# Kernel tuning notes

Measured on AMD Instinct MI355X. Metric: run time of the kernel, lower is better.

Reference implementation:

```python
import jax, jax.numpy as jnp
import numpy as np

EPS = 1e-5

def _layer_norm(x, gamma, beta):
    # LayerNorm over the last two dims [C, 128], matching nn.LayerNorm([C, 128])
    mean = jnp.mean(x, axis=(-2, -1), keepdims=True)
    var = jnp.var(x, axis=(-2, -1), keepdims=True)
    return (x - mean) * jax.lax.rsqrt(var + EPS) * gamma + beta


def setup_inputs() -> dict:
    key = jax.random.key(0)
    ks = jax.random.split(key, 7)
    B, C, N, L = 64, 1024, 128, 512
    W_SCALE = 0.02  # keep pre-softmax logits / activations in a sane range
    return {
        "X_in": jax.random.normal(ks[0], (B, C, N), jnp.float32),
        "T": jax.random.normal(ks[1], (B, C, L), jnp.float32),
        "Wq": jax.random.normal(ks[2], (C, C), jnp.float32) * W_SCALE,
        "Wk": jax.random.normal(ks[3], (C, C), jnp.float32) * W_SCALE,
        "Wv": jax.random.normal(ks[4], (C, C), jnp.float32) * W_SCALE,
        "Wf1": jax.random.normal(ks[5], (C, C), jnp.float32) * W_SCALE,
        "Wf2": jax.random.normal(ks[6], (C, C), jnp.float32) * W_SCALE,
        "gamma": jnp.ones((C, N), jnp.float32),
        "beta": jnp.zeros((C, N), jnp.float32),
    }


def reference(X_in, T, Wq, Wk, Wv, Wf1, Wf2, gamma, beta):
    C = Wq.shape[1]  # feature_map_cs (intended value of the buggy X_in.weight.shape[1])
    # 1x1 Conv1d == per-position channel matmul: weight [out, in]
    q = jnp.einsum('oc,bcn->bon', Wq, X_in)      # [B, C, N]
    k = jnp.einsum('oc,bcl->bol', Wk, T)         # [B, C, L]
    sim = jnp.einsum('bcn,bcl->bnl', q, k) / jnp.sqrt(jnp.float32(C))  # [B, N, L]
    attn = jax.nn.softmax(sim, axis=2)           # softmax over tokens L
    v = jnp.einsum('oc,bcl->bol', Wv, T)         # [B, C, L]
    ctx = jnp.einsum('bcl,bnl->bcn', v, attn)    # [B, C, N] == bmm(values, attn^T)
    X_out = _layer_norm(X_in + ctx, gamma, beta)
    h = jax.nn.relu(jnp.einsum('oc,bcn->bon', Wf1, X_out))
    ffn = jnp.einsum('oc,bcn->bon', Wf2, h)
    return _layer_norm(X_out + ffn, gamma, beta)
```

## Files before the change

kernel.cpp:

```cpp
#include <hip/hip_runtime.h>


using bf16   = __bf16;
using bf16x2 = __attribute__((ext_vector_type(2))) __bf16;
using bf16x4 = __attribute__((ext_vector_type(4))) __bf16;
using bf16x8 = __attribute__((ext_vector_type(8))) __bf16;
using f32x4  = __attribute__((ext_vector_type(4))) float;

static constexpr int  Bb = 64;
static constexpr int  Cc = 1024;
static constexpr int  Nn = 128;
static constexpr int  Ll = 512;
static constexpr long long PLANE = (long long)Cc * Nn;
static constexpr float INV_PLANE = 1.0f / 131072.0f;

__device__ __forceinline__ void gload_lds16(const void* g, void* l) {
    __builtin_amdgcn_global_load_lds(
        (__attribute__((address_space(1))) void*)g,
        (__attribute__((address_space(3))) void*)l,
        16, 0, 0);
}

__global__ void cast_w3(const float* __restrict__ a, const float* __restrict__ b,
                        const float* __restrict__ c,
                        bf16* __restrict__ oa, bf16* __restrict__ ob, bf16* __restrict__ oc) {
    const float* in; bf16* out;
    switch (blockIdx.y) {
        case 0: in = a; out = oa; break;
        case 1: in = b; out = ob; break;
        default: in = c; out = oc; break;
    }
    int i = blockIdx.x * 256 + threadIdx.x;
    float4 v = reinterpret_cast<const float4*>(in)[i];
    bf16x4 o = { (bf16)v.x, (bf16)v.y, (bf16)v.z, (bf16)v.w };
    reinterpret_cast<bf16x4*>(out)[i] = o;
}

template <bool DUAL>
__global__ void transpose_cast_f(const float* __restrict__ in, bf16* __restrict__ outT,
                                 bf16* __restrict__ outS, int R, int S) {
    __shared__ float tile[64][65];
    long long plane = (long long)R * S;
    in   += (long long)blockIdx.z * plane;
    outT += (long long)blockIdx.z * plane;
    if (DUAL) outS += (long long)blockIdx.z * plane;
    int s0 = blockIdx.x * 64, r0 = blockIdx.y * 64;
    int t = threadIdx.x;
    int rl = t >> 4;
    int sc = (t & 15) * 4;
    #pragma unroll
    for (int p = 0; p < 4; ++p) {
        int r = p * 16 + rl;
        float4 v = *(const float4*)(in + (long long)(r0 + r) * S + s0 + sc);
        *(float4*)&tile[r][sc] = v;
        if (DUAL) {
            bf16x4 o = { (bf16)v.x, (bf16)v.y, (bf16)v.z, (bf16)v.w };
            *(bf16x4*)(outS + (long long)(r0 + r) * S + s0 + sc) = o;
        }
    }
    __syncthreads();
    int sb = t >> 3;
    int rg = (t & 7) * 8;
    #pragma unroll
    for (int p = 0; p < 2; ++p) {
        int s = sb + p * 32;
        bf16x8 o;
        #pragma unroll
        for (int j = 0; j < 8; ++j) o[j] = (bf16)tile[rg + j][s];
        *(bf16x8*)(outT + (long long)(s0 + s) * R + r0 + rg) = o;
    }
}

__global__ void transpose_cast_w2(const float* __restrict__ a, bf16* __restrict__ oa,
                                  const float* __restrict__ b, bf16* __restrict__ ob) {
    __shared__ float tile[64][65];
    const float* in = blockIdx.z ? b : a;
    bf16* out       = blockIdx.z ? ob : oa;
    int s0 = blockIdx.x * 64, r0 = blockIdx.y * 64;
    int t = threadIdx.x;
    int rl = t >> 4, sc = (t & 15) * 4;
    #pragma unroll
    for (int p = 0; p < 4; ++p) {
        int r = p * 16 + rl;
        float4 v = *(const float4*)(in + (long long)(r0 + r) * Cc + s0 + sc);
        *(float4*)&tile[r][sc] = v;
    }
    __syncthreads();
    int sb = t >> 3, rg = (t & 7) * 8;
    #pragma unroll
    for (int p = 0; p < 2; ++p) {
        int s = sb + p * 32;
        bf16x8 o;
        #pragma unroll
        for (int j = 0; j < 8; ++j) o[j] = (bf16)tile[rg + j][s];
        *(bf16x8*)(out + (long long)(s0 + s) * Cc + r0 + rg) = o;
    }
}

#define GEMM_PROLOGUE_AND_LOOP(A_, Bt_, K_)                                        \
    __shared__ bf16 As[128 * 64];                                                  \
    __shared__ bf16 Bs[128 * 64];                                                  \
    const int n0   = blockIdx.x * 128;                                             \
    const int m0   = blockIdx.y * 128;                                             \
    const int t    = threadIdx.x;                                                  \
    const int lane = t & 63;                                                       \
    const int w    = t >> 6;                                                       \
    const int wr   = (w >> 1) * 64;                                                \
    const int wc   = (w & 1) * 64;                                                 \
    const int lr   = lane & 15;                                                    \
    const int hi4  = (lane >> 4) * 16;                                             \
    const int sw   = (lr & 7) << 4;                                                \
    const bf16* gA[4]; const bf16* gB[4]; int lo[4];                               \
    _Pragma("unroll")                                                              \
    for (int p = 0; p < 4; ++p) {                                                  \
        int o = w * 1024 + lane * 16 + p * 4096;                                   \
        int row = o >> 7;                                                          \
        int scol = ((o & 127) ^ ((row & 7) << 4)) >> 1;                            \
        lo[p] = o;                                                                 \
        gA[p] = A_  + (long long)(m0 + row) * K_ + scol;                           \
        gB[p] = Bt_ + (long long)(n0 + row) * K_ + scol;                           \
    }                                                                              \
    f32x4 acc[4][4] = {};                                                          \
    for (int k0 = 0; k0 < K_; k0 += 64) {                                          \
        _Pragma("unroll")                                                          \
        for (int p = 0; p < 4; ++p) gload_lds16(gA[p] + k0, (char*)As + lo[p]);    \
        _Pragma("unroll")                                                          \
        for (int p = 0; p < 4; ++p) gload_lds16(gB[p] + k0, (char*)Bs + lo[p]);    \
        __syncthreads();                                                           \
        _Pragma("unroll")                                                          \
        for (int kk = 0; kk < 2; ++kk) {                                           \
            bf16x8 af[4], bfr[4];                                                  \
            _Pragma("unroll")                                                      \
            for (int i = 0; i < 4; ++i) {                                          \
                int ra = wr + i * 16 + lr;                                         \
                int rb = wc + i * 16 + lr;                                         \
                af[i]  = *(const bf16x8*)((const char*)As +                        \
                          ((((ra << 7) + (kk << 6) + hi4)) ^ sw));                 \
                bfr[i] = *(const bf16x8*)((const char*)Bs +                        \
                          ((((rb << 7) + (kk << 6) + hi4)) ^ sw));                 \
            }                                                                      \
            _Pragma("unroll")                                                      \
            for (int mi = 0; mi < 4; ++mi)                                         \
                _Pragma("unroll")                                                  \
                for (int ni = 0; ni < 4; ++ni)                                     \
                    acc[mi][ni] = __builtin_amdgcn_mfma_f32_16x16x32_bf16(         \
                        af[mi], bfr[ni], acc[mi][ni], 0, 0, 0);                    \
        }                                                                          \
        __syncthreads();                                                           \
    }

template <typename OutT, bool RELU>
__global__ void __launch_bounds__(256, 2)
gemm_tn(const bf16* __restrict__ A, const bf16* __restrict__ Bt, OutT* __restrict__ C,
        int M, int N, int K, long long sA, long long sBt, long long sC, float scale) {
    A  += (long long)blockIdx.z * sA;
    Bt += (long long)blockIdx.z * sBt;
    C  += (long long)blockIdx.z * sC;
    GEMM_PROLOGUE_AND_LOOP(A, Bt, K)
    const int rbase = m0 + wr + (lane >> 4) * 4;
    const int cbase = n0 + wc + lr;
    #pragma unroll
    for (int mi = 0; mi < 4; ++mi)
        #pragma unroll
        for (int ni = 0; ni < 4; ++ni)
            #pragma unroll
            for (int r = 0; r < 4; ++r) {
                float v = acc[mi][ni][r] * scale;
                if (RELU) v = fmaxf(v, 0.0f);
                C[(long long)(rbase + mi * 16 + r) * N + (cbase + ni * 16)] = (OutT)v;
            }
}

__global__ void __launch_bounds__(256, 2)
gemm_sim_exp(const bf16* __restrict__ A , const bf16* __restrict__ Bt ,
             bf16* __restrict__ E, float* __restrict__ rspart, int K,
             long long sA, long long sBt) {
    A  += (long long)blockIdx.z * sA;
    Bt += (long long)blockIdx.z * sBt;
    E  += (long long)blockIdx.z * ((long long)Nn * Ll);
    GEMM_PROLOGUE_AND_LOOP(A, Bt, K)
    const int rbase = m0 + wr + (lane >> 4) * 4;
    const int cbase = n0 + wc + lr;
    __shared__ float rs[2][128];
    float psum[4][4];
    #pragma unroll
    for (int mi = 0; mi < 4; ++mi)
        #pragma unroll
        for (int r = 0; r < 4; ++r) psum[mi][r] = 0.f;
    #pragma unroll
    for (int mi = 0; mi < 4; ++mi)
        #pragma unroll
        for (int ni = 0; ni < 4; ++ni)
            #pragma unroll
            for (int r = 0; r < 4; ++r) {
                float ev = __expf(acc[mi][ni][r] * 0.03125f);
                E[(long long)(rbase + mi * 16 + r) * Ll + (cbase + ni * 16)] = (bf16)ev;
                psum[mi][r] += ev;
            }
    #pragma unroll
    for (int mi = 0; mi < 4; ++mi)
        #pragma unroll
        for (int r = 0; r < 4; ++r) {
            float v = psum[mi][r];
            v += __shfl_xor(v, 1); v += __shfl_xor(v, 2);
            v += __shfl_xor(v, 4); v += __shfl_xor(v, 8);
            psum[mi][r] = v;
        }
    if (lr == 0) {
        #pragma unroll
        for (int mi = 0; mi < 4; ++mi)
            #pragma unroll
            for (int r = 0; r < 4; ++r)
                rs[wc ? 1 : 0][wr + (lane >> 4) * 4 + mi * 16 + r] = psum[mi][r];
    }
    __syncthreads();
    if (t < 128)
        rspart[((long long)blockIdx.z * 4 + blockIdx.x) * 128 + t] = rs[0][t] + rs[1][t];
}

__global__ void __launch_bounds__(256, 2)
gemm_u_scaled(const bf16* __restrict__ A , const bf16* __restrict__ Bt ,
              bf16* __restrict__ C, const float* __restrict__ rspart, int K,
              long long sA, long long sBt, long long sC) {
    A  += (long long)blockIdx.z * sA;
    Bt += (long long)blockIdx.z * sBt;
    C  += (long long)blockIdx.z * sC;
    const float* rp = rspart + (long long)blockIdx.z * 512;
    GEMM_PROLOGUE_AND_LOOP(A, Bt, K)
    const int rbase = m0 + wr + (lane >> 4) * 4;
    const int cbase = n0 + wc + lr;
    #pragma unroll
    for (int mi = 0; mi < 4; ++mi)
        #pragma unroll
        for (int r = 0; r < 4; ++r) {
            int row = rbase + mi * 16 + r;
            float inv = 1.f / (rp[row] + rp[128 + row] + rp[256 + row] + rp[384 + row]);
            #pragma unroll
            for (int ni = 0; ni < 4; ++ni)
                C[(long long)row * Cc + (cbase + ni * 16)] = (bf16)(acc[mi][ni][r] * inv);
        }
}

__global__ void __launch_bounds__(256, 2)
gemm_ctx_ln1(const bf16* __restrict__ A , const bf16* __restrict__ Bt ,
             const float* __restrict__ X, float* __restrict__ Z1, float* __restrict__ partials,
             int K, long long sBt) {
    const int N = Nn;
    Bt += (long long)blockIdx.z * sBt;
    X  += (long long)blockIdx.z * PLANE;
    Z1 += (long long)blockIdx.z * PLANE;
    GEMM_PROLOGUE_AND_LOOP(A, Bt, K)
    const int rbase = m0 + wr + (lane >> 4) * 4;
    const int cbase = n0 + wc + lr;
    float s = 0.f, ss = 0.f;
    #pragma unroll
    for (int mi = 0; mi < 4; ++mi)
        #pragma unroll
        for (int ni = 0; ni < 4; ++ni)
            #pragma unroll
            for (int r = 0; r < 4; ++r) {
                long long idx = (long long)(rbase + mi * 16 + r) * N + (cbase + ni * 16);
                float zv = acc[mi][ni][r] + X[idx];
                Z1[idx] = zv;
                s += zv; ss += zv * zv;
            }
    #pragma unroll
    for (int off = 32; off; off >>= 1) { s += __shfl_xor(s, off); ss += __shfl_xor(ss, off); }
    __shared__ float red[8];
    if (lane == 0) { red[w] = s; red[4 + w] = ss; }
    __syncthreads();
    if (t == 0) {
        float S = red[0] + red[1] + red[2] + red[3];
        float SS = red[4] + red[5] + red[6] + red[7];
        float* p = partials + ((long long)blockIdx.z * 8 + blockIdx.y) * 2;
        p[0] = S; p[1] = SS;
    }
}

__global__ void __launch_bounds__(256, 2)
gemm_ffn_ln2(const bf16* __restrict__ A , const bf16* __restrict__ Bt ,
             const float* __restrict__ Z1, const float* __restrict__ pp1,
             const float* __restrict__ gamma, const float* __restrict__ beta,
             float* __restrict__ Z2, float* __restrict__ partials,
             int K, long long sA) {
    A  += (long long)blockIdx.z * sA;
    Z1 += (long long)blockIdx.z * PLANE;
    Z2 += (long long)blockIdx.z * PLANE;
    float S1 = 0.f, SS1 = 0.f;
    #pragma unroll
    for (int j = 0; j < 8; ++j) {
        S1  += pp1[((long long)blockIdx.z * 8 + j) * 2];
        SS1 += pp1[((long long)blockIdx.z * 8 + j) * 2 + 1];
    }
    const float mean1 = S1 * INV_PLANE;
    const float rstd1 = rsqrtf(SS1 * INV_PLANE - mean1 * mean1 + 1e-5f);
    GEMM_PROLOGUE_AND_LOOP(A, Bt, K)
    const int rbase = m0 + wr + (lane >> 4) * 4;
    const int cbase = n0 + wc + lr;
    float s = 0.f, ss = 0.f;
    #pragma unroll
    for (int mi = 0; mi < 4; ++mi)
        #pragma unroll
        for (int ni = 0; ni < 4; ++ni) {
            long long a = (long long)(cbase + ni * 16) * Nn + rbase + mi * 16;
            float4 z1v = *(const float4*)(Z1 + a);
            float4 g  = *(const float4*)(gamma + a);
            float4 be = *(const float4*)(beta + a);
            float4 xo = {(z1v.x - mean1) * rstd1 * g.x + be.x,
                         (z1v.y - mean1) * rstd1 * g.y + be.y,
                         (z1v.z - mean1) * rstd1 * g.z + be.z,
                         (z1v.w - mean1) * rstd1 * g.w + be.w};
            float4 zv = { acc[mi][ni][0] + xo.x, acc[mi][ni][1] + xo.y,
                          acc[mi][ni][2] + xo.z, acc[mi][ni][3] + xo.w };
            *(float4*)(Z2 + a) = zv;
            s  += zv.x + zv.y + zv.z + zv.w;
            ss += zv.x * zv.x + zv.y * zv.y + zv.z * zv.z + zv.w * zv.w;
        }
    #pragma unroll
    for (int off = 32; off; off >>= 1) { s += __shfl_xor(s, off); ss += __shfl_xor(ss, off); }
    __shared__ float red[8];
    if (lane == 0) { red[w] = s; red[4 + w] = ss; }
    __syncthreads();
    if (t == 0) {
        float S = red[0] + red[1] + red[2] + red[3];
        float SS = red[4] + red[5] + red[6] + red[7];
        float* p = partials + ((long long)blockIdx.z * 8 + blockIdx.x) * 2;
        p[0] = S; p[1] = SS;
    }
}

__global__ void ln1_norm_transpose(const float* __restrict__ Z1, const float* __restrict__ partials,
                                   const float* __restrict__ gamma, const float* __restrict__ beta,
                                   bf16* __restrict__ XoutT) {
    int b = blockIdx.z;
    float S = 0.f, SS = 0.f;
    #pragma unroll
    for (int j = 0; j < 8; ++j) {
        S  += partials[((long long)b * 8 + j) * 2];
        SS += partials[((long long)b * 8 + j) * 2 + 1];
    }
    float mean = S * INV_PLANE;
    float var  = SS * INV_PLANE - mean * mean;
    float rstd = rsqrtf(var + 1e-5f);
    __shared__ float tile[64][65];
    long long base = (long long)b * PLANE;
    int n0 = blockIdx.x * 64, c0 = blockIdx.y * 64;
    int t = threadIdx.x;
    int rl = t >> 4;
    int sc = (t & 15) * 4;
    #pragma unroll
    for (int p = 0; p < 4; ++p) {
        int r = p * 16 + rl;
        long long idx = (long long)(c0 + r) * Nn + n0 + sc;
        float4 z  = *(const float4*)(Z1 + base + idx);
        float4 g  = *(const float4*)(gamma + idx);
        float4 be = *(const float4*)(beta + idx);
        float4 o = {(z.x - mean) * rstd * g.x + be.x, (z.y - mean) * rstd * g.y + be.y,
                    (z.z - mean) * rstd * g.z + be.z, (z.w - mean) * rstd * g.w + be.w};
        *(float4*)&tile[r][sc] = o;
    }
    __syncthreads();
    int sb = t >> 3;
    int rg = (t & 7) * 8;
    #pragma unroll
    for (int p = 0; p < 2; ++p) {
        int n = sb + p * 32;
        bf16x8 o;
        #pragma unroll
        for (int j = 0; j < 8; ++j) o[j] = (bf16)tile[rg + j][n];
        *(bf16x8*)(XoutT + base + (long long)(n0 + n) * Cc + c0 + rg) = o;
    }
}

__global__ void ln2_final(const float* __restrict__ Z2, const float* __restrict__ partials,
                          const float* __restrict__ gamma, const float* __restrict__ beta,
                          float* __restrict__ out) {
    int b = blockIdx.y;
    float S = 0.f, SS = 0.f;
    #pragma unroll
    for (int j = 0; j < 8; ++j) {
        S  += partials[((long long)b * 8 + j) * 2];
        SS += partials[((long long)b * 8 + j) * 2 + 1];
    }
    float mean = S * INV_PLANE;
    float var  = SS * INV_PLANE - mean * mean;
    float rstd = rsqrtf(var + 1e-5f);
    long long base = (long long)b * PLANE;
    int i = (blockIdx.x * 256 + threadIdx.x) * 4;
    float4 z  = *(const float4*)(Z2 + base + i);
    float4 g  = *(const float4*)(gamma + i);
    float4 be = *(const float4*)(beta + i);
    float4 o = {(z.x - mean) * rstd * g.x + be.x, (z.y - mean) * rstd * g.y + be.y,
                (z.z - mean) * rstd * g.z + be.z, (z.w - mean) * rstd * g.w + be.w};
    *(float4*)(out + base + i) = o;
}

extern "C" void kernel_launch(void* const* d_in, const int* in_sizes, int n_in,
                              void* d_out, int out_size, void* d_ws, size_t ws_size,
                              hipStream_t stream) {
    const float* X   = (const float*)d_in[0];
    const float* T   = (const float*)d_in[1];
    const float* Wq  = (const float*)d_in[2];
    const float* Wk  = (const float*)d_in[3];
    const float* Wv  = (const float*)d_in[4];
    const float* Wf1 = (const float*)d_in[5];
    const float* Wf2 = (const float*)d_in[6];
    const float* gamma = (const float*)d_in[7];
    const float* beta  = (const float*)d_in[8];
    float* out = (float*)d_out;
    char* ws = (char*)d_ws;
    const size_t MB = 1ull << 20;

    bf16* WvB  = (bf16*)(ws + 0 * MB);
    bf16* Wf1B = (bf16*)(ws + 2 * MB);
    bf16* Wf2B = (bf16*)(ws + 4 * MB);
    bf16* WqT  = (bf16*)(ws + 6 * MB);
    bf16* WkT  = (bf16*)(ws + 8 * MB);
    bf16* G2   = (bf16*)(ws + 10 * MB);
    bf16* Xt   = (bf16*)(ws + 12 * MB);
    bf16* Tt   = (bf16*)(ws + 28 * MB);
    float* Z1  = (float*)(ws + 28 * MB);
    bf16* Tb   = (bf16*)(ws + 92 * MB);
    bf16* XoutT= (bf16*)(ws + 92 * MB);
    bf16* hT   = (bf16*)(ws + 108 * MB);
    bf16* e    = (bf16*)(ws + 156 * MB);
    float* Z2  = (float*)(ws + 156 * MB);
    bf16* E    = (bf16*)(ws + 188 * MB);
    bf16* u    = (bf16*)(ws + 196 * MB);
    float* pp1 = (float*)(ws + 212 * MB);
    float* pp2 = (float*)(ws + 212 * MB + 65536);
    float* rsp = (float*)(ws + 213 * MB);

    dim3 blk256(256);

    cast_w3<<<dim3(Cc * Cc / 4 / 256, 3), blk256, 0, stream>>>(
        Wv, Wf1, Wf2, WvB, Wf1B, Wf2B);
    transpose_cast_w2<<<dim3(16, 16, 2), blk256, 0, stream>>>(Wq, WqT, Wk, WkT);
    transpose_cast_f<false><<<dim3(Nn / 64, Cc / 64, Bb), blk256, 0, stream>>>(X, Xt, nullptr, Cc, Nn);
    transpose_cast_f<true><<<dim3(Ll / 64, Cc / 64, Bb), blk256, 0, stream>>>(T, Tt, Tb, Cc, Ll);

    gemm_tn<bf16, false><<<dim3(8, 8, 1), blk256, 0, stream>>>(
        WkT, WqT, G2, Cc, Cc, Cc, 0, 0, 0, 1.f);
    gemm_tn<bf16, false><<<dim3(8, 1, Bb), blk256, 0, stream>>>(
        Xt, G2, e, Nn, Cc, Cc, (long long)Nn * Cc, 0, (long long)Nn * Cc, 1.f);
    gemm_sim_exp<<<dim3(4, 1, Bb), blk256, 0, stream>>>(
        e, Tt, E, rsp, Cc, (long long)Nn * Cc, (long long)Ll * Cc);
    gemm_u_scaled<<<dim3(8, 1, Bb), blk256, 0, stream>>>(
        E, Tb, u, rsp, Ll, (long long)Nn * Ll, (long long)Cc * Ll, (long long)Nn * Cc);
    gemm_ctx_ln1<<<dim3(1, 8, Bb), blk256, 0, stream>>>(
        WvB, u, X, Z1, pp1, Cc, (long long)Nn * Cc);
    ln1_norm_transpose<<<dim3(Nn / 64, Cc / 64, Bb), blk256, 0, stream>>>(
        Z1, pp1, gamma, beta, XoutT);
    gemm_tn<bf16, true><<<dim3(8, 1, Bb), blk256, 0, stream>>>(
        XoutT, Wf1B, hT, Nn, Cc, Cc, (long long)Nn * Cc, 0, (long long)Nn * Cc, 1.f);
    gemm_ffn_ln2<<<dim3(8, 1, Bb), blk256, 0, stream>>>(
        hT, Wf2B, Z1, pp1, gamma, beta, Z2, pp2, Cc, (long long)Nn * Cc);
    ln2_final<<<dim3(128, Bb), blk256, 0, stream>>>(Z2, pp2, gamma, beta, out);
}
```

Before: 292.8 us.

## Merge prep kernels, double-buffer GEMM LDS tiles, store LN intermediates as bf16

Folds the four weight/input cast and transpose kernels into one prep_all launch that dispatches by block index. Double-buffers the shared A/B tiles in the GEMM macro so the next K-tile's global-to-LDS load is issued while the current tile is computed. Stores the LN1 and LN2 pre-normalization intermediates Z1/Z2 as bf16 instead of fp32, halving their traffic at some cost in precision. Doubling LDS to 64KB per block may lower occupancy for the kernels that request two blocks per CU.

```diff
diff --git a/kernel.cpp b/kernel.cpp
--- a/kernel.cpp
+++ b/kernel.cpp
@@ -2,7 +2,6 @@
 
 
 using bf16   = __bf16;
-using bf16x2 = __attribute__((ext_vector_type(2))) __bf16;
 using bf16x4 = __attribute__((ext_vector_type(4))) __bf16;
 using bf16x8 = __attribute__((ext_vector_type(8))) __bf16;
 using f32x4  = __attribute__((ext_vector_type(4))) float;
@@ -21,31 +20,44 @@
         16, 0, 0);
 }
 
-__global__ void cast_w3(const float* __restrict__ a, const float* __restrict__ b,
-                        const float* __restrict__ c,
-                        bf16* __restrict__ oa, bf16* __restrict__ ob, bf16* __restrict__ oc) {
-    const float* in; bf16* out;
-    switch (blockIdx.y) {
-        case 0: in = a; out = oa; break;
-        case 1: in = b; out = ob; break;
-        default: in = c; out = oc; break;
-    }
-    int i = blockIdx.x * 256 + threadIdx.x;
-    float4 v = reinterpret_cast<const float4*>(in)[i];
-    bf16x4 o = { (bf16)v.x, (bf16)v.y, (bf16)v.z, (bf16)v.w };
-    reinterpret_cast<bf16x4*>(out)[i] = o;
-}
-
-template <bool DUAL>
-__global__ void transpose_cast_f(const float* __restrict__ in, bf16* __restrict__ outT,
-                                 bf16* __restrict__ outS, int R, int S) {
+__global__ void __launch_bounds__(256)
+prep_all(const float* __restrict__ Wv, const float* __restrict__ Wf1,
+         const float* __restrict__ Wf2, const float* __restrict__ Wq,
+         const float* __restrict__ Wk, const float* __restrict__ X,
+         const float* __restrict__ T,
+         bf16* __restrict__ WvB, bf16* __restrict__ Wf1B, bf16* __restrict__ Wf2B,
+         bf16* __restrict__ WqT, bf16* __restrict__ WkT,
+         bf16* __restrict__ Xt, bf16* __restrict__ Tt, bf16* __restrict__ Tb) {
     __shared__ float tile[64][65];
+    const int bx = blockIdx.x;
+    const int t  = threadIdx.x;
+    if (bx < 3072) {
+        const float* in = bx < 1024 ? Wv : (bx < 2048 ? Wf1 : Wf2);
+        bf16* out       = bx < 1024 ? WvB : (bx < 2048 ? Wf1B : Wf2B);
+        int i = (bx & 1023) * 256 + t;
+        float4 v = reinterpret_cast<const float4*>(in)[i];
+        bf16x4 o = { (bf16)v.x, (bf16)v.y, (bf16)v.z, (bf16)v.w };
+        reinterpret_cast<bf16x4*>(out)[i] = o;
+        return;
+    }
+    const float* in; bf16* outT; bf16* outS = nullptr;
+    int R, S, bxx, byy, bz = 0;
+    if (bx < 3584) {
+        int j = bx - 3072;
+        in = (j >= 256) ? Wk : Wq; outT = (j >= 256) ? WkT : WqT;
+        R = Cc; S = Cc; j &= 255; bxx = j & 15; byy = j >> 4;
+    } else if (bx < 5632) {
+        int j = bx - 3584; bz = j >> 5; j &= 31;
+        bxx = j & 1; byy = j >> 1; in = X; outT = Xt; R = Cc; S = Nn;
+    } else {
+        int j = bx - 5632; bz = j >> 7; j &= 127;
+        bxx = j & 7; byy = j >> 3; in = T; outT = Tt; outS = Tb; R = Cc; S = Ll;
+    }
     long long plane = (long long)R * S;
-    in   += (long long)blockIdx.z * plane;
-    outT += (long long)blockIdx.z * plane;
-    if (DUAL) outS += (long long)blockIdx.z * plane;
-    int s0 = blockIdx.x * 64, r0 = blockIdx.y * 64;
-    int t = threadIdx.x;
+    in   += (long long)bz * plane;
+    outT += (long long)bz * plane;
+    if (outS) outS += (long long)bz * plane;
+    int s0 = bxx * 64, r0 = byy * 64;
     int rl = t >> 4;
     int sc = (t & 15) * 4;
     #pragma unroll
@@ -53,7 +65,7 @@
         int r = p * 16 + rl;
         float4 v = *(const float4*)(in + (long long)(r0 + r) * S + s0 + sc);
         *(float4*)&tile[r][sc] = v;
-        if (DUAL) {
+        if (outS) {
             bf16x4 o = { (bf16)v.x, (bf16)v.y, (bf16)v.z, (bf16)v.w };
             *(bf16x4*)(outS + (long long)(r0 + r) * S + s0 + sc) = o;
         }
@@ -71,35 +83,9 @@
     }
 }
 
-__global__ void transpose_cast_w2(const float* __restrict__ a, bf16* __restrict__ oa,
-                                  const float* __restrict__ b, bf16* __restrict__ ob) {
-    __shared__ float tile[64][65];
-    const float* in = blockIdx.z ? b : a;
-    bf16* out       = blockIdx.z ? ob : oa;
-    int s0 = blockIdx.x * 64, r0 = blockIdx.y * 64;
-    int t = threadIdx.x;
-    int rl = t >> 4, sc = (t & 15) * 4;
-    #pragma unroll
-    for (int p = 0; p < 4; ++p) {
-        int r = p * 16 + rl;
-        float4 v = *(const float4*)(in + (long long)(r0 + r) * Cc + s0 + sc);
-        *(float4*)&tile[r][sc] = v;
-    }
-    __syncthreads();
-    int sb = t >> 3, rg = (t & 7) * 8;
-    #pragma unroll
-    for (int p = 0; p < 2; ++p) {
-        int s = sb + p * 32;
-        bf16x8 o;
-        #pragma unroll
-        for (int j = 0; j < 8; ++j) o[j] = (bf16)tile[rg + j][s];
-        *(bf16x8*)(out + (long long)(s0 + s) * Cc + r0 + rg) = o;
-    }
-}
-
 #define GEMM_PROLOGUE_AND_LOOP(A_, Bt_, K_)                                        \
-    __shared__ bf16 As[128 * 64];                                                  \
-    __shared__ bf16 Bs[128 * 64];                                                  \
+    __shared__ bf16 As[2][128 * 64];                                               \
+    __shared__ bf16 Bs[2][128 * 64];                                               \
     const int n0   = blockIdx.x * 128;                                             \
     const int m0   = blockIdx.y * 128;                                             \
     const int t    = threadIdx.x;                                                  \
@@ -121,12 +107,23 @@
         gB[p] = Bt_ + (long long)(n0 + row) * K_ + scol;                           \
     }                                                                              \
     f32x4 acc[4][4] = {};                                                          \
-    for (int k0 = 0; k0 < K_; k0 += 64) {                                          \
-        _Pragma("unroll")                                                          \
-        for (int p = 0; p < 4; ++p) gload_lds16(gA[p] + k0, (char*)As + lo[p]);    \
-        _Pragma("unroll")                                                          \
-        for (int p = 0; p < 4; ++p) gload_lds16(gB[p] + k0, (char*)Bs + lo[p]);    \
-        __syncthreads();                                                           \
+    const int NT_ = K_ / 64;                                                       \
+    _Pragma("unroll")                                                              \
+    for (int p = 0; p < 4; ++p) gload_lds16(gA[p], (char*)As[0] + lo[p]);          \
+    _Pragma("unroll")                                                              \
+    for (int p = 0; p < 4; ++p) gload_lds16(gB[p], (char*)Bs[0] + lo[p]);          \
+    __syncthreads();                                                               \
+    int cur_ = 0;                                                                  \
+    for (int kt = 0; kt < NT_; ++kt) {                                             \
+        if (kt + 1 < NT_) {                                                        \
+            _Pragma("unroll")                                                      \
+            for (int p = 0; p < 4; ++p)                                            \
+                gload_lds16(gA[p] + (kt + 1) * 64, (char*)As[cur_ ^ 1] + lo[p]);   \
+            _Pragma("unroll")                                                      \
+            for (int p = 0; p < 4; ++p)                                            \
+                gload_lds16(gB[p] + (kt + 1) * 64, (char*)Bs[cur_ ^ 1] + lo[p]);   \
+        }                                                                          \
+        const bf16* As_ = As[cur_]; const bf16* Bs_ = Bs[cur_];                    \
         _Pragma("unroll")                                                          \
         for (int kk = 0; kk < 2; ++kk) {                                           \
             bf16x8 af[4], bfr[4];                                                  \
@@ -134,9 +131,9 @@
             for (int i = 0; i < 4; ++i) {                                          \
                 int ra = wr + i * 16 + lr;                                         \
                 int rb = wc + i * 16 + lr;                                         \
-                af[i]  = *(const bf16x8*)((const char*)As +                        \
+                af[i]  = *(const bf16x8*)((const char*)As_ +                       \
                           ((((ra << 7) + (kk << 6) + hi4)) ^ sw));                 \
-                bfr[i] = *(const bf16x8*)((const char*)Bs +                        \
+                bfr[i] = *(const bf16x8*)((const char*)Bs_ +                       \
                           ((((rb << 7) + (kk << 6) + hi4)) ^ sw));                 \
             }                                                                      \
             _Pragma("unroll")                                                      \
@@ -147,6 +144,7 @@
                         af[mi], bfr[ni], acc[mi][ni], 0, 0, 0);                    \
         }                                                                          \
         __syncthreads();                                                           \
+        cur_ ^= 1;                                                                 \
     }
 
 template <typename OutT, bool RELU>
@@ -243,7 +241,7 @@
 
 __global__ void __launch_bounds__(256, 2)
 gemm_ctx_ln1(const bf16* __restrict__ A , const bf16* __restrict__ Bt ,
-             const float* __restrict__ X, float* __restrict__ Z1, float* __restrict__ partials,
+             const float* __restrict__ X, bf16* __restrict__ Z1, float* __restrict__ partials,
              int K, long long sBt) {
     const int N = Nn;
     Bt += (long long)blockIdx.z * sBt;
@@ -261,7 +259,7 @@
             for (int r = 0; r < 4; ++r) {
                 long long idx = (long long)(rbase + mi * 16 + r) * N + (cbase + ni * 16);
                 float zv = acc[mi][ni][r] + X[idx];
-                Z1[idx] = zv;
+                Z1[idx] = (bf16)zv;
                 s += zv; ss += zv * zv;
             }
     #pragma unroll
@@ -279,9 +277,9 @@
 
 __global__ void __launch_bounds__(256, 2)
 gemm_ffn_ln2(const bf16* __restrict__ A , const bf16* __restrict__ Bt ,
-             const float* __restrict__ Z1, const float* __restrict__ pp1,
+             const bf16* __restrict__ Z1, const float* __restrict__ pp1,
              const float* __restrict__ gamma, const float* __restrict__ beta,
-             float* __restrict__ Z2, float* __restrict__ partials,
+             bf16* __restrict__ Z2, float* __restrict__ partials,
              int K, long long sA) {
     A  += (long long)blockIdx.z * sA;
     Z1 += (long long)blockIdx.z * PLANE;
@@ -303,18 +301,19 @@
         #pragma unroll
         for (int ni = 0; ni < 4; ++ni) {
             long long a = (long long)(cbase + ni * 16) * Nn + rbase + mi * 16;
-            float4 z1v = *(const float4*)(Z1 + a);
+            bf16x4 z1v = *(const bf16x4*)(Z1 + a);
             float4 g  = *(const float4*)(gamma + a);
             float4 be = *(const float4*)(beta + a);
-            float4 xo = {(z1v.x - mean1) * rstd1 * g.x + be.x,
-                         (z1v.y - mean1) * rstd1 * g.y + be.y,
-                         (z1v.z - mean1) * rstd1 * g.z + be.z,
-                         (z1v.w - mean1) * rstd1 * g.w + be.w};
-            float4 zv = { acc[mi][ni][0] + xo.x, acc[mi][ni][1] + xo.y,
-                          acc[mi][ni][2] + xo.z, acc[mi][ni][3] + xo.w };
-            *(float4*)(Z2 + a) = zv;
-            s  += zv.x + zv.y + zv.z + zv.w;
-            ss += zv.x * zv.x + zv.y * zv.y + zv.z * zv.z + zv.w * zv.w;
+            float x0 = ((float)z1v[0] - mean1) * rstd1 * g.x + be.x;
+            float x1 = ((float)z1v[1] - mean1) * rstd1 * g.y + be.y;
+            float x2 = ((float)z1v[2] - mean1) * rstd1 * g.z + be.z;
+            float x3 = ((float)z1v[3] - mean1) * rstd1 * g.w + be.w;
+            float z0 = acc[mi][ni][0] + x0, z1 = acc[mi][ni][1] + x1;
+            float z2 = acc[mi][ni][2] + x2, z3 = acc[mi][ni][3] + x3;
+            bf16x4 zo = { (bf16)z0, (bf16)z1, (bf16)z2, (bf16)z3 };
+            *(bf16x4*)(Z2 + a) = zo;
+            s  += z0 + z1 + z2 + z3;
+            ss += z0 * z0 + z1 * z1 + z2 * z2 + z3 * z3;
         }
     #pragma unroll
     for (int off = 32; off; off >>= 1) { s += __shfl_xor(s, off); ss += __shfl_xor(ss, off); }
@@ -329,7 +328,7 @@
     }
 }
 
-__global__ void ln1_norm_transpose(const float* __restrict__ Z1, const float* __restrict__ partials,
+__global__ void ln1_norm_transpose(const bf16* __restrict__ Z1, const float* __restrict__ partials,
                                    const float* __restrict__ gamma, const float* __restrict__ beta,
                                    bf16* __restrict__ XoutT) {
     int b = blockIdx.z;
@@ -352,11 +351,13 @@
     for (int p = 0; p < 4; ++p) {
         int r = p * 16 + rl;
         long long idx = (long long)(c0 + r) * Nn + n0 + sc;
-        float4 z  = *(const float4*)(Z1 + base + idx);
+        bf16x4 z  = *(const bf16x4*)(Z1 + base + idx);
         float4 g  = *(const float4*)(gamma + idx);
         float4 be = *(const float4*)(beta + idx);
-        float4 o = {(z.x - mean) * rstd * g.x + be.x, (z.y - mean) * rstd * g.y + be.y,
-                    (z.z - mean) * rstd * g.z + be.z, (z.w - mean) * rstd * g.w + be.w};
+        float4 o = {((float)z[0] - mean) * rstd * g.x + be.x,
+                    ((float)z[1] - mean) * rstd * g.y + be.y,
+                    ((float)z[2] - mean) * rstd * g.z + be.z,
+                    ((float)z[3] - mean) * rstd * g.w + be.w};
         *(float4*)&tile[r][sc] = o;
     }
     __syncthreads();
@@ -372,7 +373,7 @@
     }
 }
 
-__global__ void ln2_final(const float* __restrict__ Z2, const float* __restrict__ partials,
+__global__ void ln2_final(const bf16* __restrict__ Z2, const float* __restrict__ partials,
                           const float* __restrict__ gamma, const float* __restrict__ beta,
                           float* __restrict__ out) {
     int b = blockIdx.y;
@@ -386,13 +387,18 @@
     float var  = SS * INV_PLANE - mean * mean;
     float rstd = rsqrtf(var + 1e-5f);
     long long base = (long long)b * PLANE;
-    int i = (blockIdx.x * 256 + threadIdx.x) * 4;
-    float4 z  = *(const float4*)(Z2 + base + i);
-    float4 g  = *(const float4*)(gamma + i);
-    float4 be = *(const float4*)(beta + i);
-    float4 o = {(z.x - mean) * rstd * g.x + be.x, (z.y - mean) * rstd * g.y + be.y,
-                (z.z - mean) * rstd * g.z + be.z, (z.w - mean) * rstd * g.w + be.w};
-    *(float4*)(out + base + i) = o;
+    int i = (blockIdx.x * 256 + threadIdx.x) * 8;
+    bf16x8 z = *(const bf16x8*)(Z2 + base + i);
+    #pragma unroll
+    for (int h = 0; h < 2; ++h) {
+        float4 g  = *(const float4*)(gamma + i + h * 4);
+        float4 be = *(const float4*)(beta + i + h * 4);
+        float4 o = {((float)z[h * 4 + 0] - mean) * rstd * g.x + be.x,
+                    ((float)z[h * 4 + 1] - mean) * rstd * g.y + be.y,
+                    ((float)z[h * 4 + 2] - mean) * rstd * g.z + be.z,
+                    ((float)z[h * 4 + 3] - mean) * rstd * g.w + be.w};
+        *(float4*)(out + base + i + h * 4) = o;
+    }
 }
 
 extern "C" void kernel_launch(void* const* d_in, const int* in_sizes, int n_in,
@@ -419,12 +425,12 @@
     bf16* G2   = (bf16*)(ws + 10 * MB);
     bf16* Xt   = (bf16*)(ws + 12 * MB);
     bf16* Tt   = (bf16*)(ws + 28 * MB);
-    float* Z1  = (float*)(ws + 28 * MB);
+    bf16* Z1   = (bf16*)(ws + 28 * MB);
     bf16* Tb   = (bf16*)(ws + 92 * MB);
     bf16* XoutT= (bf16*)(ws + 92 * MB);
     bf16* hT   = (bf16*)(ws + 108 * MB);
     bf16* e    = (bf16*)(ws + 156 * MB);
-    float* Z2  = (float*)(ws + 156 * MB);
+    bf16* Z2   = (bf16*)(ws + 156 * MB);
     bf16* E    = (bf16*)(ws + 188 * MB);
     bf16* u    = (bf16*)(ws + 196 * MB);
     float* pp1 = (float*)(ws + 212 * MB);
@@ -433,11 +439,8 @@
 
     dim3 blk256(256);
 
-    cast_w3<<<dim3(Cc * Cc / 4 / 256, 3), blk256, 0, stream>>>(
-        Wv, Wf1, Wf2, WvB, Wf1B, Wf2B);
-    transpose_cast_w2<<<dim3(16, 16, 2), blk256, 0, stream>>>(Wq, WqT, Wk, WkT);
-    transpose_cast_f<false><<<dim3(Nn / 64, Cc / 64, Bb), blk256, 0, stream>>>(X, Xt, nullptr, Cc, Nn);
-    transpose_cast_f<true><<<dim3(Ll / 64, Cc / 64, Bb), blk256, 0, stream>>>(T, Tt, Tb, Cc, Ll);
+    prep_all<<<dim3(13824), blk256, 0, stream>>>(
+        Wv, Wf1, Wf2, Wq, Wk, X, T, WvB, Wf1B, Wf2B, WqT, WkT, Xt, Tt, Tb);
 
     gemm_tn<bf16, false><<<dim3(8, 8, 1), blk256, 0, stream>>>(
         WkT, WqT, G2, Cc, Cc, Cc, 0, 0, 0, 1.f);
@@ -455,5 +458,5 @@
         XoutT, Wf1B, hT, Nn, Cc, Cc, (long long)Nn * Cc, 0, (long long)Nn * Cc, 1.f);
     gemm_ffn_ln2<<<dim3(8, 1, Bb), blk256, 0, stream>>>(
         hT, Wf2B, Z1, pp1, gamma, beta, Z2, pp2, Cc, (long long)Nn * Cc);
-    ln2_final<<<dim3(128, Bb), blk256, 0, stream>>>(Z2, pp2, gamma, beta, out);
-}
+    ln2_final<<<dim3(64, Bb), blk256, 0, stream>>>(Z2, pp2, gamma, beta, out);
+}
```

Measured after the change: 291.8 us. Within noise of the previous version (-0.3%).
